# Kernel tuning notes

Hardware: AMD Instinct MI355X
Metric: run time of the kernel (lower is better)

Reference implementation:

```python
import jax, jax.numpy as jnp
from jax import lax
import numpy as np

# Model hyperparameters (match init_kwargs)
NUM_STEPS = 6
N_ETYPES = 8
D_IN = 128
D_OUT = 128
B, N, E = 32, 1024, 262144  # graphs, nodes per graph, total edges


def setup_inputs() -> dict:
    key = jax.random.key(0)
    ks = jax.random.split(key, 24)
    s = 0.05  # param scale for numeric stability over 6 GRU steps
    inp = {
        "h": jax.random.normal(ks[0], (B, N, D_IN), jnp.float32),
        "src": jax.random.randint(ks[1], (E,), 0, B * N, jnp.int32),
        "dst": jax.random.randint(ks[2], (E,), 0, B * N, jnp.int32),
        "etype": jax.random.randint(ks[3], (E,), 0, N_ETYPES, jnp.int32),
        "W_msg": jax.random.normal(ks[4], (N_ETYPES, D_OUT, D_OUT), jnp.float32) * s,
        "b_msg": jax.random.normal(ks[5], (N_ETYPES, D_OUT), jnp.float32) * s,
        "w_ih": jax.random.normal(ks[6], (3 * D_OUT, D_OUT), jnp.float32) * s,
        "w_hh": jax.random.normal(ks[7], (3 * D_OUT, D_OUT), jnp.float32) * s,
        "b_ih": jax.random.normal(ks[8], (3 * D_OUT,), jnp.float32) * s,
        "b_hh": jax.random.normal(ks[9], (3 * D_OUT,), jnp.float32) * s,
        "conv1_w": jax.random.normal(ks[10], (D_OUT, D_OUT, 3), jnp.float32) * s,
        "conv1_b": jax.random.normal(ks[11], (D_OUT,), jnp.float32) * s,
        "conv2_w": jax.random.normal(ks[12], (D_OUT, D_OUT, 1), jnp.float32) * s,
        "conv2_b": jax.random.normal(ks[13], (D_OUT,), jnp.float32) * s,
        "cc1_w": jax.random.normal(ks[14], (D_IN + D_OUT, D_IN + D_OUT, 3), jnp.float32) * s,
        "cc1_b": jax.random.normal(ks[15], (D_IN + D_OUT,), jnp.float32) * s,
        "cc2_w": jax.random.normal(ks[16], (D_IN + D_OUT, D_IN + D_OUT, 1), jnp.float32) * s,
        "cc2_b": jax.random.normal(ks[17], (D_IN + D_OUT,), jnp.float32) * s,
        "mlp_y_w": jax.random.normal(ks[18], (1, D_OUT), jnp.float32) * s,
        "mlp_y_b": jax.random.normal(ks[19], (1,), jnp.float32) * s,
        "mlp_z_w": jax.random.normal(ks[20], (1, D_IN + D_OUT), jnp.float32) * s,
        "mlp_z_b": jax.random.normal(ks[21], (1,), jnp.float32) * s,
    }
    return inp


def _conv1d(x, w, b):
    # x: [B, C_in, L], w: [C_out, C_in, K]
    y = lax.conv_general_dilated(x, w, (1,), "VALID",
                                 dimension_numbers=("NCW", "OIW", "NCW"))
    return y + b[None, :, None]


def _maxpool1d(x, k, stride):
    return lax.reduce_window(x, -jnp.inf, lax.max,
                             (1, 1, k), (1, 1, stride), "VALID")


def _ggnn(h0, src, dst, etype, W_msg, b_msg, w_ih, w_hh, b_ih, b_hh):
    # h0: [BN, D_OUT] (in_feats == out_feats so no zero-padding needed)
    n_nodes = h0.shape[0]

    def step(h, _):
        # transform each node by every etype weight: [BN, T, O]
        t = jnp.einsum("nd,tod->nto", h, W_msg) + b_msg
        m = t[src, etype]                                   # [E, O] gather
        a = jax.ops.segment_sum(m, dst, num_segments=n_nodes)  # scatter-add
        # torch.nn.GRUCell(a, h)
        gi = a @ w_ih.T + b_ih
        gh = h @ w_hh.T + b_hh
        i_r, i_z, i_n = jnp.split(gi, 3, axis=-1)
        h_r, h_z, h_n = jnp.split(gh, 3, axis=-1)
        r = jax.nn.sigmoid(i_r + h_r)
        z = jax.nn.sigmoid(i_z + h_z)
        n = jnp.tanh(i_n + r * h_n)
        return (1.0 - z) * n + z * h, None

    h_final, _ = lax.scan(step, h0, None, length=NUM_STEPS)
    return h_final


def reference(h, src, dst, etype, W_msg, b_msg, w_ih, w_hh, b_ih, b_hh,
              conv1_w, conv1_b, conv2_w, conv2_b, cc1_w, cc1_b, cc2_w, cc2_b,
              mlp_y_w, mlp_y_b, mlp_z_w, mlp_z_b):
    b, n, d = h.shape
    x = h.reshape(b * n, d)
    h_next = _ggnn(x, src, dst, etype, W_msg, b_msg, w_ih, w_hh, b_ih, b_hh)
    h_i = h_next.reshape(b, n, -1)                   # [B, N, O]
    c_i = jnp.concatenate([h_i, h], axis=-1)          # [B, N, O+D]

    Y_1 = _maxpool1d(jax.nn.relu(_conv1d(h_i.transpose(0, 2, 1), conv1_w, conv1_b)), 3, 2)
    Y_2 = _maxpool1d(jax.nn.relu(_conv1d(Y_1, conv2_w, conv2_b)), 2, 2).transpose(0, 2, 1)
    Z_1 = _maxpool1d(jax.nn.relu(_conv1d(c_i.transpose(0, 2, 1), cc1_w, cc1_b)), 3, 2)
    Z_2 = _maxpool1d(jax.nn.relu(_conv1d(Z_1, cc2_w, cc2_b)), 2, 2).transpose(0, 2, 1)

    before_avg = (Y_2 @ mlp_y_w.T + mlp_y_b) * (Z_2 @ mlp_z_w.T + mlp_z_b)  # [B, L, 1]
    avg = before_avg.mean(axis=1)                     # [B, 1]
    return jax.nn.sigmoid(avg).squeeze(-1)            # [B]
```

## Files before the change

kernel.cpp:

```cpp
#include <hip/hip_runtime.h>
#include <math.h>

#define BB 32
#define NNODE 1024
#define BN 32768
#define NE 262144
#define DD 128
#define NT 8
#define NSTEPS 6

typedef __attribute__((ext_vector_type(8))) short bf16x8;
typedef __attribute__((ext_vector_type(4))) float f32x4;

static __device__ __forceinline__ float4 ld4(const float* p) { return *(const float4*)p; }
static __device__ __forceinline__ float sigmoidf_(float x) { return 1.f / (1.f + expf(-x)); }
static __device__ __forceinline__ unsigned f2b(float f) {
    unsigned u = __float_as_uint(f);
    return (u + 0x7FFFu + ((u >> 16) & 1u)) >> 16;
}
static __device__ __forceinline__ float b2f(unsigned short b) {
    return __uint_as_float(((unsigned)b) << 16);
}
static __device__ __forceinline__ unsigned pk(float a, float b) {
    return f2b(a) | (f2b(b) << 16);
}
static __device__ __forceinline__ unsigned bmax2(unsigned a, unsigned b) {
    unsigned ah = a & 0xFFFF0000u, bh = b & 0xFFFF0000u;
    unsigned al = a & 0x0000FFFFu, bl = b & 0x0000FFFFu;
    return (ah > bh ? ah : bh) | (al > bl ? al : bl);
}
static __device__ __forceinline__ uint4 bmax4(uint4 a, uint4 b) {
    return make_uint4(bmax2(a.x, b.x), bmax2(a.y, b.y), bmax2(a.z, b.z), bmax2(a.w, b.w));
}

static constexpr size_t OFF_HCUR = 0;
static constexpr size_t OFF_HBF  = OFF_HCUR + (size_t)BN * DD * 4;
static constexpr size_t OFF_CNT  = OFF_HBF  + (size_t)BN * DD * 2;
static constexpr size_t OFF_DOFF = OFF_CNT  + (size_t)BN * NT * 4;
static constexpr size_t OFF_DBLK = OFF_DOFF + (size_t)BN * 4;
static constexpr size_t OFF_VTOF = OFF_DBLK + 512;
static constexpr size_t OFF_VTCU = OFF_VTOF + (size_t)BN * NT * 4;
static constexpr size_t OFF_SRC2 = OFF_VTCU + (size_t)BN * NT * 4;
static constexpr size_t OFF_WMB  = OFF_SRC2 + (size_t)NE * 4;
static constexpr size_t OFF_WIHB = OFF_WMB  + (size_t)NT * DD * DD * 2;
static constexpr size_t OFF_WHHB = OFF_WIHB + (size_t)3 * DD * DD * 2;
static constexpr size_t OFF_W1PY = OFF_WHHB + (size_t)3 * DD * DD * 2;
static constexpr size_t OFF_W1PZ = OFF_W1PY + (size_t)3 * 128 * 128 * 2;
static constexpr size_t OFF_W2YB = OFF_W1PZ + (size_t)3 * 256 * 256 * 2;
static constexpr size_t OFF_W2ZB = OFF_W2YB + (size_t)128 * 128 * 2;
static constexpr size_t OFF_ABF  = OFF_W2ZB + (size_t)256 * 256 * 2;
static constexpr size_t OFF_UN   = OFF_ABF  + (size_t)BN * DD * 2;
static constexpr size_t OFF_U1Y  = OFF_UN;
static constexpr size_t OFF_U1Z  = OFF_U1Y + (size_t)32 * 1024 * 128 * 2;
static constexpr size_t OFF_QY   = OFF_U1Z + (size_t)32 * 1024 * 256 * 2;
static constexpr size_t OFF_QZ   = OFF_QY  + (size_t)32 * 255 * 128 * 4;
static constexpr size_t WS_NEED  = OFF_QZ  + (size_t)32 * 255 * 256 * 4;

#define PREP_BLOCKS 5616
__global__ void k_prep(const float* __restrict__ h_in, float* __restrict__ hcur,
                       unsigned short* __restrict__ hbf,
                       const float* __restrict__ Wmsg, unsigned short* __restrict__ wmb,
                       const float* __restrict__ wih, unsigned short* __restrict__ wihb,
                       const float* __restrict__ whh, unsigned short* __restrict__ whhb,
                       const float* __restrict__ c2w, unsigned short* __restrict__ w2yb,
                       const float* __restrict__ z2w, unsigned short* __restrict__ w2zb,
                       const float* __restrict__ c1w, unsigned short* __restrict__ w1py,
                       const float* __restrict__ z1w, unsigned short* __restrict__ w1pz,
                       int* __restrict__ cnt)
{
    int blk = blockIdx.x, tid = threadIdx.x;
    if (blk < 4096) {
        int i = blk * 256 + tid;
        float4 v = ((const float4*)h_in)[i];
        ((float4*)hcur)[i] = v;
        ((uint2*)hbf)[i] = make_uint2(pk(v.x, v.y), pk(v.z, v.w));
    } else if (blk < 4224) {
        int i = (blk - 4096) * 256 + tid;
        float4 v = ((const float4*)Wmsg)[i];
        ((uint2*)wmb)[i] = make_uint2(pk(v.x, v.y), pk(v.z, v.w));
    } else if (blk < 4272) {
        int i = (blk - 4224) * 256 + tid;
        float4 v = ((const float4*)wih)[i];
        ((uint2*)wihb)[i] = make_uint2(pk(v.x, v.y), pk(v.z, v.w));
    } else if (blk < 4320) {
        int i = (blk - 4272) * 256 + tid;
        float4 v = ((const float4*)whh)[i];
        ((uint2*)whhb)[i] = make_uint2(pk(v.x, v.y), pk(v.z, v.w));
    } else if (blk < 4336) {
        int i = (blk - 4320) * 256 + tid;
        float4 v = ((const float4*)c2w)[i];
        ((uint2*)w2yb)[i] = make_uint2(pk(v.x, v.y), pk(v.z, v.w));
    } else if (blk < 4400) {
        int i = (blk - 4336) * 256 + tid;
        float4 v = ((const float4*)z2w)[i];
        ((uint2*)w2zb)[i] = make_uint2(pk(v.x, v.y), pk(v.z, v.w));
    } else if (blk < 4592) {
        int g = (blk - 4400) * 256 + tid;
        int k = g >> 14, rem = g & 16383;
        w1py[g] = (unsigned short)f2b(c1w[(size_t)rem * 3 + k]);
    } else if (blk < 5360) {
        int g = (blk - 4592) * 256 + tid;
        int k = g >> 16, rem = g & 65535;
        w1pz[g] = (unsigned short)f2b(z1w[(size_t)rem * 3 + k]);
    } else {
        ((uint4*)cnt)[(blk - 5360) * 256 + tid] = make_uint4(0, 0, 0, 0);
    }
}


__global__ void k_hist(const int* __restrict__ et, const int* __restrict__ dst,
                       int* __restrict__ cnt)
{
    int base = blockIdx.x * 1024, tid = threadIdx.x;
    for (int k = 0; k < 4; ++k) {
        int e = base + tid + k * 256;
        atomicAdd(&cnt[(size_t)dst[e] * NT + et[e]], 1);
    }
}

__global__ void k_degA(const int* __restrict__ cnt, int* __restrict__ doff,
                       int* __restrict__ dblk)
{
    __shared__ int ps[256];
    int tid = threadIdx.x;
    int v = blockIdx.x * 256 + tid;
    const int* cv = cnt + (size_t)v * NT;
    int d = 0;
#pragma unroll
    for (int t = 0; t < NT; ++t) d += cv[t];
    ps[tid] = d;
    __syncthreads();
    for (int off = 1; off < 256; off <<= 1) {
        int x = 0;
        if (tid >= off) x = ps[tid - off];
        __syncthreads();
        ps[tid] += x;
        __syncthreads();
    }
    doff[v] = ps[tid] - d;
    if (tid == 255) dblk[blockIdx.x] = ps[255];
}

__global__ void k_scan2(int* __restrict__ dblk)
{
    __shared__ int s[128];
    int tid = threadIdx.x;
    s[tid] = dblk[tid];
    __syncthreads();
    if (tid == 0) {
        int run = 0;
        for (int i = 0; i < 128; ++i) { int x = s[i]; s[i] = run; run += x; }
    }
    __syncthreads();
    dblk[tid] = s[tid];
}

__global__ void k_degB(const int* __restrict__ cnt, const int* __restrict__ doff,
                       const int* __restrict__ dblk,
                       int* __restrict__ vtoff, int* __restrict__ vtcur)
{
    int v = blockIdx.x * 256 + threadIdx.x;
    int run = doff[v] + dblk[blockIdx.x];
    const int* cv = cnt + (size_t)v * NT;
    int* vo = vtoff + (size_t)v * NT;
    int* vc = vtcur + (size_t)v * NT;
#pragma unroll
    for (int t = 0; t < NT; ++t) { vo[t] = run; vc[t] = run; run += cv[t]; }
}

__global__ void k_scatter(const int* __restrict__ src, const int* __restrict__ dst,
                          const int* __restrict__ et,
                          int* __restrict__ vtcur, int* __restrict__ ssrc2)
{
    int e = blockIdx.x * 256 + threadIdx.x;
    int slot = atomicAdd(&vtcur[(size_t)dst[e] * NT + et[e]], 1);
    ssrc2[slot] = src[e];
}


__launch_bounds__(256, 3)
__global__ void k_msgagg(const int* __restrict__ ssrc2, const int* __restrict__ vtoff,
                         const int* __restrict__ cnt,
                         const unsigned short* __restrict__ hbf,
                         const unsigned short* __restrict__ wmb,
                         const float* __restrict__ bmsg,
                         unsigned short* __restrict__ abf)
{
    __shared__ __align__(16) unsigned short As[64 * 128];
    __shared__ __align__(16) unsigned short Ws[128 * 128];
    __shared__ float bm[NT * DD];
    int m0 = blockIdx.x * 64;
    int tid = threadIdx.x;
    *(float4*)&bm[tid * 4] = ld4(bmsg + tid * 4);
    int lane = tid & 63, wv = tid >> 6;
    int wm = (wv >> 1) * 32, wn = (wv & 1) * 64;
    int lr = lane & 15, lk = lane >> 4;
    f32x4 acc[2][4];
#pragma unroll
    for (int i = 0; i < 2; ++i)
#pragma unroll
        for (int j = 0; j < 4; ++j) acc[i][j] = (f32x4){0.f, 0.f, 0.f, 0.f};

    int rA = tid >> 2, qA = tid & 3;
    unsigned bA = rA * 256 + qA * 64, swA = (rA & 7) << 4;
    int rW = tid >> 1, hW = tid & 1;
    unsigned bW = rW * 256 + hW * 128, swW = (rW & 7) << 4;
    int node = m0 + rA;

#pragma unroll
    for (int t = 0; t < NT; ++t) {
        __syncthreads();
        {
            int start = vtoff[(size_t)node * NT + t];
            int cv    = cnt[(size_t)node * NT + t];
            if (cv == 1) {
                const uint4* sp = (const uint4*)(hbf + (size_t)ssrc2[start] * DD + qA * 32);
#pragma unroll
                for (int c = 0; c < 4; ++c)
                    *(uint4*)((char*)As + ((bA + c * 16) ^ swA)) = sp[c];
            } else if (cv == 0) {
                uint4 z = make_uint4(0, 0, 0, 0);
#pragma unroll
                for (int c = 0; c < 4; ++c)
                    *(uint4*)((char*)As + ((bA + c * 16) ^ swA)) = z;
            } else {
                float ac[32];
#pragma unroll
                for (int j = 0; j < 32; ++j) ac[j] = 0.f;
                for (int i = 0; i < cv; ++i) {
                    const uint4* sp = (const uint4*)(hbf + (size_t)ssrc2[start + i] * DD + qA * 32);
#pragma unroll
                    for (int c = 0; c < 4; ++c) {
                        uint4 w = sp[c];
                        ac[c * 8 + 0] += b2f((unsigned short)(w.x & 0xFFFF));
                        ac[c * 8 + 1] += b2f((unsigned short)(w.x >> 16));
                        ac[c * 8 + 2] += b2f((unsigned short)(w.y & 0xFFFF));
                        ac[c * 8 + 3] += b2f((unsigned short)(w.y >> 16));
                        ac[c * 8 + 4] += b2f((unsigned short)(w.z & 0xFFFF));
                        ac[c * 8 + 5] += b2f((unsigned short)(w.z >> 16));
                        ac[c * 8 + 6] += b2f((unsigned short)(w.w & 0xFFFF));
                        ac[c * 8 + 7] += b2f((unsigned short)(w.w >> 16));
                    }
                }
#pragma unroll
                for (int c = 0; c < 4; ++c) {
                    uint4 o = make_uint4(pk(ac[c * 8 + 0], ac[c * 8 + 1]), pk(ac[c * 8 + 2], ac[c * 8 + 3]),
                                         pk(ac[c * 8 + 4], ac[c * 8 + 5]), pk(ac[c * 8 + 6], ac[c * 8 + 7]));
                    *(uint4*)((char*)As + ((bA + c * 16) ^ swA)) = o;
                }
            }
        }
        {
            const uint4* wp = (const uint4*)(wmb + ((size_t)t * DD + rW) * DD + hW * 64);
#pragma unroll
            for (int c = 0; c < 8; ++c)
                *(uint4*)((char*)Ws + ((bW + c * 16) ^ swW)) = wp[c];
        }
        __syncthreads();
#pragma unroll
        for (int kc = 0; kc < 4; ++kc) {
            int cb = kc * 64 + lk * 16;
            bf16x8 af[2], bfv[4];
#pragma unroll
            for (int mi = 0; mi < 2; ++mi) {
                int row = wm + mi * 16 + lr;
                af[mi] = *(const bf16x8*)((const char*)As + ((row * 256 + cb) ^ ((row & 7) << 4)));
            }
#pragma unroll
            for (int ni = 0; ni < 4; ++ni) {
                int row = wn + ni * 16 + lr;
                bfv[ni] = *(const bf16x8*)((const char*)Ws + ((row * 256 + cb) ^ ((row & 7) << 4)));
            }
#pragma unroll
            for (int mi = 0; mi < 2; ++mi)
#pragma unroll
                for (int ni = 0; ni < 4; ++ni)
                    acc[mi][ni] = __builtin_amdgcn_mfma_f32_16x16x32_bf16(af[mi], bfv[ni], acc[mi][ni], 0, 0, 0);
        }
    }
#pragma unroll
    for (int mi = 0; mi < 2; ++mi)
#pragma unroll
        for (int rg = 0; rg < 4; ++rg) {
            int v = m0 + wm + mi * 16 + lk * 4 + rg;
            const int* cvp = cnt + (size_t)v * NT;
            float c0 = (float)cvp[0], c1 = (float)cvp[1], c2 = (float)cvp[2], c3 = (float)cvp[3];
            float c4 = (float)cvp[4], c5 = (float)cvp[5], c6 = (float)cvp[6], c7 = (float)cvp[7];
#pragma unroll
            for (int ni = 0; ni < 4; ++ni) {
                int col = wn + ni * 16 + lr;
                float bias = c0 * bm[col] + c1 * bm[DD + col] + c2 * bm[2 * DD + col] + c3 * bm[3 * DD + col]
                           + c4 * bm[4 * DD + col] + c5 * bm[5 * DD + col] + c6 * bm[6 * DD + col] + c7 * bm[7 * DD + col];
                abf[(size_t)v * DD + col] = (unsigned short)f2b(acc[mi][ni][rg] + bias);
            }
        }
}


__launch_bounds__(512, 2)
__global__ void k_gru(const unsigned short* __restrict__ abf, float* __restrict__ h,
                      unsigned short* __restrict__ hbf,
                      const unsigned short* __restrict__ wihb, const unsigned short* __restrict__ whhb,
                      const float* __restrict__ bih, const float* __restrict__ bhh)
{
    __shared__ __align__(16) unsigned short Xs[128 * 128];
    __shared__ __align__(16) unsigned short Ws2[128 * 128];
    int m0 = blockIdx.x * 128;
    int tid = threadIdx.x;
    int lane = tid & 63, wv = tid >> 6;
    int wm = (wv >> 1) * 32, wn = (wv & 1) * 64;
    int lr = lane & 15, lk = lane >> 4;
    f32x4 aR[2][4], aZ[2][4], aI[2][4], aH[2][4];
#pragma unroll
    for (int i = 0; i < 2; ++i)
#pragma unroll
        for (int j = 0; j < 4; ++j) {
            aR[i][j] = (f32x4){0.f, 0.f, 0.f, 0.f};
            aZ[i][j] = (f32x4){0.f, 0.f, 0.f, 0.f};
            aI[i][j] = (f32x4){0.f, 0.f, 0.f, 0.f};
            aH[i][j] = (f32x4){0.f, 0.f, 0.f, 0.f};
        }
    int rx = tid >> 2, qx = tid & 3;
    unsigned bx = rx * 256 + qx * 64, swx = (rx & 7) << 4;
#pragma unroll
    for (int pass = 0; pass < 2; ++pass) {
        const unsigned short* X = pass ? hbf : abf;
        const unsigned short* W = pass ? whhb : wihb;
#pragma unroll
        for (int g = 0; g < 3; ++g) {
            __syncthreads();
            if (g == 0) {
                const uint4* sp = (const uint4*)(X + (size_t)(m0 + rx) * DD + qx * 32);
#pragma unroll
                for (int c = 0; c < 4; ++c)
                    *(uint4*)((char*)Xs + ((bx + c * 16) ^ swx)) = sp[c];
            }
            {
                const uint4* wp = (const uint4*)(W + (size_t)(g * DD + rx) * DD + qx * 32);
#pragma unroll
                for (int c = 0; c < 4; ++c)
                    *(uint4*)((char*)Ws2 + ((bx + c * 16) ^ swx)) = wp[c];
            }
            __syncthreads();
#pragma unroll
            for (int kc = 0; kc < 4; ++kc) {
                int cb = kc * 64 + lk * 16;
                bf16x8 af[2], bfv[4];
#pragma unroll
                for (int mi = 0; mi < 2; ++mi) {
                    int row = wm + mi * 16 + lr;
                    af[mi] = *(const bf16x8*)((const char*)Xs + ((row * 256 + cb) ^ ((row & 7) << 4)));
                }
#pragma unroll
                for (int ni = 0; ni < 4; ++ni) {
                    int row = wn + ni * 16 + lr;
                    bfv[ni] = *(const bf16x8*)((const char*)Ws2 + ((row * 256 + cb) ^ ((row & 7) << 4)));
                }
#pragma unroll
                for (int mi = 0; mi < 2; ++mi)
#pragma unroll
                    for (int ni = 0; ni < 4; ++ni) {
                        if (g == 0)
                            aR[mi][ni] = __builtin_amdgcn_mfma_f32_16x16x32_bf16(af[mi], bfv[ni], aR[mi][ni], 0, 0, 0);
                        else if (g == 1)
                            aZ[mi][ni] = __builtin_amdgcn_mfma_f32_16x16x32_bf16(af[mi], bfv[ni], aZ[mi][ni], 0, 0, 0);
                        else if (pass == 0)
                            aI[mi][ni] = __builtin_amdgcn_mfma_f32_16x16x32_bf16(af[mi], bfv[ni], aI[mi][ni], 0, 0, 0);
                        else
                            aH[mi][ni] = __builtin_amdgcn_mfma_f32_16x16x32_bf16(af[mi], bfv[ni], aH[mi][ni], 0, 0, 0);
                    }
            }
        }
    }
#pragma unroll
    for (int ni = 0; ni < 4; ++ni) {
        int col = wn + ni * 16 + lr;
        float br_ = bih[col] + bhh[col];
        float bz_ = bih[DD + col] + bhh[DD + col];
        float bin_ = bih[2 * DD + col], bhn_ = bhh[2 * DD + col];
#pragma unroll
        for (int mi = 0; mi < 2; ++mi)
#pragma unroll
            for (int rg = 0; rg < 4; ++rg) {
                int v = m0 + wm + mi * 16 + lk * 4 + rg;
                float rr = sigmoidf_(aR[mi][ni][rg] + br_);
                float zz = sigmoidf_(aZ[mi][ni][rg] + bz_);
                float nn = tanhf(aI[mi][ni][rg] + bin_ + rr * (aH[mi][ni][rg] + bhn_));
                float hold = h[(size_t)v * DD + col];
                float hnew = (1.f - zz) * nn + zz * hold;
                h[(size_t)v * DD + col] = hnew;
                hbf[(size_t)v * DD + col] = (unsigned short)f2b(hnew);
            }
    }
}


template <int CIN>
__launch_bounds__(256, 2)
__global__ void k_conv1m(const unsigned short* __restrict__ hbf, const float* __restrict__ h0,
                         const unsigned short* __restrict__ w1p, const float* __restrict__ bias,
                         unsigned short* __restrict__ U1)
{
    __shared__ __align__(16) unsigned short As[128 * 64];
    __shared__ __align__(16) unsigned short Ws[128 * 64];
    int p0 = blockIdx.x * 128, b = blockIdx.y, n0 = blockIdx.z * 128;
    int tid = threadIdx.x;
    int lane = tid & 63, wv = tid >> 6;
    int wm = (wv >> 1) * 64, wn = (wv & 1) * 64;
    int lr = lane & 15, lk = lane >> 4;
    f32x4 acc[4][4];
#pragma unroll
    for (int i = 0; i < 4; ++i)
#pragma unroll
        for (int j = 0; j < 4; ++j) acc[i][j] = (f32x4){0.f, 0.f, 0.f, 0.f};

    int r = tid >> 1, halfc = tid & 1;
    unsigned boff = r * 128 + halfc * 64;
    unsigned sw = (r & 7) << 4;
#pragma unroll
    for (int k = 0; k < 3; ++k) {
        for (int c0 = 0; c0 < CIN; c0 += 64) {
            __syncthreads();
            {
                int row = p0 + k + r; if (row > NNODE - 1) row = NNODE - 1;
                int ci = c0 + halfc * 32;
                if (CIN == 128 || ci < 128) {
                    const uint4* sp = (const uint4*)(hbf + ((size_t)(b * NNODE + row)) * DD + ci);
#pragma unroll
                    for (int c = 0; c < 4; ++c)
                        *(uint4*)((char*)As + ((boff + c * 16) ^ sw)) = sp[c];
                } else {
                    const float4* sp = (const float4*)(h0 + ((size_t)(b * NNODE + row)) * DD + (ci - 128));
#pragma unroll
                    for (int c = 0; c < 4; ++c) {
                        float4 v0 = sp[2 * c], v1 = sp[2 * c + 1];
                        *(uint4*)((char*)As + ((boff + c * 16) ^ sw)) =
                            make_uint4(pk(v0.x, v0.y), pk(v0.z, v0.w), pk(v1.x, v1.y), pk(v1.z, v1.w));
                    }
                }
            }
            {
                const uint4* wp = (const uint4*)(w1p + ((size_t)k * CIN + n0 + r) * CIN + c0 + halfc * 32);
#pragma unroll
                for (int c = 0; c < 4; ++c)
                    *(uint4*)((char*)Ws + ((boff + c * 16) ^ sw)) = wp[c];
            }
            __syncthreads();
#pragma unroll
            for (int kc = 0; kc < 2; ++kc) {
                int cb = kc * 64 + lk * 16;
                bf16x8 af[4], bfv[4];
#pragma unroll
                for (int mi = 0; mi < 4; ++mi) {
                    int row = wm + mi * 16 + lr;
                    af[mi] = *(const bf16x8*)((const char*)As + ((row * 128 + cb) ^ ((row & 7) << 4)));
                }
#pragma unroll
                for (int ni = 0; ni < 4; ++ni) {
                    int row = wn + ni * 16 + lr;
                    bfv[ni] = *(const bf16x8*)((const char*)Ws + ((row * 128 + cb) ^ ((row & 7) << 4)));
                }
#pragma unroll
                for (int mi = 0; mi < 4; ++mi)
#pragma unroll
                    for (int ni = 0; ni < 4; ++ni)
                        acc[mi][ni] = __builtin_amdgcn_mfma_f32_16x16x32_bf16(af[mi], bfv[ni], acc[mi][ni], 0, 0, 0);
            }
        }
    }
#pragma unroll
    for (int ni = 0; ni < 4; ++ni) {
        int co = n0 + wn + ni * 16 + lr;
        float bs = bias[co];
#pragma unroll
        for (int mi = 0; mi < 4; ++mi)
#pragma unroll
            for (int rg = 0; rg < 4; ++rg) {
                int pos = p0 + wm + mi * 16 + lk * 4 + rg;
                if (pos < NNODE - 2) {
                    float v = fmaxf(0.f, acc[mi][ni][rg] + bs);
                    U1[((size_t)b * NNODE + pos) * CIN + co] = (unsigned short)f2b(v);
                }
            }
    }
}


template <int CIN>
__launch_bounds__(256, 2)
__global__ void k_conv2m(const unsigned short* __restrict__ U1, const unsigned short* __restrict__ w2b,
                         const float* __restrict__ bias, float* __restrict__ Q)
{
    __shared__ __align__(16) unsigned short As[128 * 64];
    __shared__ __align__(16) unsigned short Ws[128 * 64];
    int m0 = blockIdx.x * 128, b = blockIdx.y, n0 = blockIdx.z * 128;
    int tid = threadIdx.x;
    int lane = tid & 63, wv = tid >> 6;
    int wm = (wv >> 1) * 64, wn = (wv & 1) * 64;
    int lr = lane & 15, lk = lane >> 4;
    f32x4 acc[4][4];
#pragma unroll
    for (int i = 0; i < 4; ++i)
#pragma unroll
        for (int j = 0; j < 4; ++j) acc[i][j] = (f32x4){0.f, 0.f, 0.f, 0.f};

    int r = tid >> 1, halfc = tid & 1;
    unsigned boff = r * 128 + halfc * 64;
    unsigned sw = (r & 7) << 4;
    for (int c0 = 0; c0 < CIN; c0 += 64) {
        __syncthreads();
        {
            int pr = 2 * (m0 + r);
            int r0 = pr, r1 = pr + 1, r2v = pr + 2;
            if (r2v > NNODE - 1) r2v = NNODE - 1;
            if (r1 > NNODE - 1) r1 = NNODE - 1;
            int ci = c0 + halfc * 32;
            const unsigned short* bp = U1 + (size_t)b * NNODE * CIN + ci;
            const uint4* p0q = (const uint4*)(bp + (size_t)r0 * CIN);
            const uint4* p1q = (const uint4*)(bp + (size_t)r1 * CIN);
            const uint4* p2q = (const uint4*)(bp + (size_t)r2v * CIN);
#pragma unroll
            for (int c = 0; c < 4; ++c) {
                uint4 mm = bmax4(bmax4(p0q[c], p1q[c]), p2q[c]);
                *(uint4*)((char*)As + ((boff + c * 16) ^ sw)) = mm;
            }
        }
        {
            const uint4* wp = (const uint4*)(w2b + (size_t)(n0 + r) * CIN + c0 + halfc * 32);
#pragma unroll
            for (int c = 0; c < 4; ++c)
                *(uint4*)((char*)Ws + ((boff + c * 16) ^ sw)) = wp[c];
        }
        __syncthreads();
#pragma unroll
        for (int kc = 0; kc < 2; ++kc) {
            int cb = kc * 64 + lk * 16;
            bf16x8 af[4], bfv[4];
#pragma unroll
            for (int mi = 0; mi < 4; ++mi) {
                int row = wm + mi * 16 + lr;
                af[mi] = *(const bf16x8*)((const char*)As + ((row * 128 + cb) ^ ((row & 7) << 4)));
            }
#pragma unroll
            for (int ni = 0; ni < 4; ++ni) {
                int row = wn + ni * 16 + lr;
                bfv[ni] = *(const bf16x8*)((const char*)Ws + ((row * 128 + cb) ^ ((row & 7) << 4)));
            }
#pragma unroll
            for (int mi = 0; mi < 4; ++mi)
#pragma unroll
                for (int ni = 0; ni < 4; ++ni)
                    acc[mi][ni] = __builtin_amdgcn_mfma_f32_16x16x32_bf16(af[mi], bfv[ni], acc[mi][ni], 0, 0, 0);
        }
    }
#pragma unroll
    for (int ni = 0; ni < 4; ++ni) {
        int co = n0 + wn + ni * 16 + lr;
        float bs = bias[co];
#pragma unroll
        for (int mi = 0; mi < 4; ++mi) {
            int l0 = m0 + wm + mi * 16 + lk * 4;
            float v0 = fmaxf(0.f, acc[mi][ni][0] + bs);
            float v1 = fmaxf(0.f, acc[mi][ni][1] + bs);
            float v2 = fmaxf(0.f, acc[mi][ni][2] + bs);
            float v3 = fmaxf(0.f, acc[mi][ni][3] + bs);
            int jq = l0 >> 1;
            if (jq < 255)     Q[((size_t)b * 255 + jq) * CIN + co]     = fmaxf(v0, v1);
            if (jq + 1 < 255) Q[((size_t)b * 255 + jq + 1) * CIN + co] = fmaxf(v2, v3);
        }
    }
}


__launch_bounds__(256)
__global__ void k_final(const float* __restrict__ QY, const float* __restrict__ QZ,
                        const float* __restrict__ wy, const float* __restrict__ by,
                        const float* __restrict__ wz, const float* __restrict__ bz,
                        float* __restrict__ out)
{
    int b = blockIdx.x, tid = threadIdx.x;
    float p = 0.f;
    if (tid < 255) {
        const float* qy = QY + ((size_t)(b * 255 + tid)) * 128;
        const float* qz = QZ + ((size_t)(b * 255 + tid)) * 256;
        float dy = 0.f, dz = 0.f;
        for (int c = 0; c < 128; c += 4) {
            float4 q = ld4(qy + c), wv = ld4(wy + c);
            dy += q.x * wv.x + q.y * wv.y + q.z * wv.z + q.w * wv.w;
        }
        for (int c = 0; c < 256; c += 4) {
            float4 q = ld4(qz + c), wv = ld4(wz + c);
            dz += q.x * wv.x + q.y * wv.y + q.z * wv.z + q.w * wv.w;
        }
        p = (dy + by[0]) * (dz + bz[0]);
    }
    __shared__ float red[4];
    for (int off = 32; off > 0; off >>= 1) p += __shfl_down(p, off);
    if ((tid & 63) == 0) red[tid >> 6] = p;
    __syncthreads();
    if (tid == 0) {
        float s = red[0] + red[1] + red[2] + red[3];
        out[b] = 1.f / (1.f + expf(-s / 255.f));
    }
}


extern "C" void kernel_launch(void* const* d_in, const int* in_sizes, int n_in,
                              void* d_out, int out_size, void* d_ws, size_t ws_size,
                              hipStream_t stream)
{
    const float* h_in = (const float*)d_in[0];
    const int* src = (const int*)d_in[1];
    const int* dst = (const int*)d_in[2];
    const int* et  = (const int*)d_in[3];
    const float* Wmsg = (const float*)d_in[4];
    const float* bmsg = (const float*)d_in[5];
    const float* wih = (const float*)d_in[6];
    const float* whh = (const float*)d_in[7];
    const float* bih = (const float*)d_in[8];
    const float* bhh = (const float*)d_in[9];
    const float* c1w = (const float*)d_in[10];
    const float* c1b = (const float*)d_in[11];
    const float* c2w = (const float*)d_in[12];
    const float* c2b = (const float*)d_in[13];
    const float* z1w = (const float*)d_in[14];
    const float* z1b = (const float*)d_in[15];
    const float* z2w = (const float*)d_in[16];
    const float* z2b = (const float*)d_in[17];
    const float* wy  = (const float*)d_in[18];
    const float* by  = (const float*)d_in[19];
    const float* wz  = (const float*)d_in[20];
    const float* bz  = (const float*)d_in[21];
    float* out = (float*)d_out;

    if (ws_size < WS_NEED) return;

    char* ws = (char*)d_ws;
    float* hcur = (float*)(ws + OFF_HCUR);
    unsigned short* hbf  = (unsigned short*)(ws + OFF_HBF);
    int*   cnt   = (int*)(ws + OFF_CNT);
    int*   doff  = (int*)(ws + OFF_DOFF);
    int*   dblk  = (int*)(ws + OFF_DBLK);
    int*   vtoff = (int*)(ws + OFF_VTOF);
    int*   vtcur = (int*)(ws + OFF_VTCU);
    int*   ssrc2 = (int*)(ws + OFF_SRC2);
    unsigned short* wmb  = (unsigned short*)(ws + OFF_WMB);
    unsigned short* wihb = (unsigned short*)(ws + OFF_WIHB);
    unsigned short* whhb = (unsigned short*)(ws + OFF_WHHB);
    unsigned short* w1py = (unsigned short*)(ws + OFF_W1PY);
    unsigned short* w1pz = (unsigned short*)(ws + OFF_W1PZ);
    unsigned short* w2yb = (unsigned short*)(ws + OFF_W2YB);
    unsigned short* w2zb = (unsigned short*)(ws + OFF_W2ZB);
    unsigned short* abf  = (unsigned short*)(ws + OFF_ABF);
    unsigned short* U1Y  = (unsigned short*)(ws + OFF_U1Y);
    unsigned short* U1Z  = (unsigned short*)(ws + OFF_U1Z);
    float* QY   = (float*)(ws + OFF_QY);
    float* QZ   = (float*)(ws + OFF_QZ);

    k_prep<<<PREP_BLOCKS, 256, 0, stream>>>(h_in, hcur, hbf, Wmsg, wmb, wih, wihb, whh, whhb,
                                            c2w, w2yb, z2w, w2zb, c1w, w1py, z1w, w1pz, cnt);

    k_hist<<<256, 256, 0, stream>>>(et, dst, cnt);
    k_degA<<<128, 256, 0, stream>>>(cnt, doff, dblk);
    k_scan2<<<1, 128, 0, stream>>>(dblk);
    k_degB<<<128, 256, 0, stream>>>(cnt, doff, dblk, vtoff, vtcur);
    k_scatter<<<1024, 256, 0, stream>>>(src, dst, et, vtcur, ssrc2);

    for (int s = 0; s < NSTEPS; ++s) {
        k_msgagg<<<BN / 64, 256, 0, stream>>>(ssrc2, vtoff, cnt, hbf, wmb, bmsg, abf);
        k_gru<<<BN / 128, 512, 0, stream>>>(abf, hcur, hbf, wihb, whhb, bih, bhh);
    }

    k_conv1m<128><<<dim3(8, 32, 1), 256, 0, stream>>>(hbf, h_in, w1py, c1b, U1Y);
    k_conv2m<128><<<dim3(4, 32, 1), 256, 0, stream>>>(U1Y, w2yb, c2b, QY);
    k_conv1m<256><<<dim3(8, 32, 2), 256, 0, stream>>>(hbf, h_in, w1pz, z1b, U1Z);
    k_conv2m<256><<<dim3(4, 32, 2), 256, 0, stream>>>(U1Z, w2zb, z2b, QZ);
    k_final<<<32, 256, 0, stream>>>(QY, QZ, wy, by, wz, bz, out);
}
```

Baseline: 611.7 us.

## Halve msgagg node tile and prefetch per-type edge sources up front

The message-aggregation kernel now handles 32 nodes per block instead of 64, with 8 threads per node row, and launches twice as many blocks. Before the type loop it loads all per-type offsets and counts as vector loads, then prefetches the first two source indices per type. This is meant to raise parallelism and hide the latency of the dependent gather loads. The cost is that each block reloads the full per-type weight matrices for half as many rows, which doubles weight traffic per node, and register pressure goes up.

```diff
diff --git a/kernel.cpp b/kernel.cpp
--- a/kernel.cpp
+++ b/kernel.cpp
@@ -31,6 +31,16 @@
 }
 static __device__ __forceinline__ uint4 bmax4(uint4 a, uint4 b) {
     return make_uint4(bmax2(a.x, b.x), bmax2(a.y, b.y), bmax2(a.z, b.z), bmax2(a.w, b.w));
+}
+static __device__ __forceinline__ void upacc(float* ac, uint4 w0, uint4 w1) {
+    ac[0] += b2f((unsigned short)(w0.x & 0xFFFF)); ac[1] += b2f((unsigned short)(w0.x >> 16));
+    ac[2] += b2f((unsigned short)(w0.y & 0xFFFF)); ac[3] += b2f((unsigned short)(w0.y >> 16));
+    ac[4] += b2f((unsigned short)(w0.z & 0xFFFF)); ac[5] += b2f((unsigned short)(w0.z >> 16));
+    ac[6] += b2f((unsigned short)(w0.w & 0xFFFF)); ac[7] += b2f((unsigned short)(w0.w >> 16));
+    ac[8] += b2f((unsigned short)(w1.x & 0xFFFF)); ac[9] += b2f((unsigned short)(w1.x >> 16));
+    ac[10] += b2f((unsigned short)(w1.y & 0xFFFF)); ac[11] += b2f((unsigned short)(w1.y >> 16));
+    ac[12] += b2f((unsigned short)(w1.z & 0xFFFF)); ac[13] += b2f((unsigned short)(w1.z >> 16));
+    ac[14] += b2f((unsigned short)(w1.w & 0xFFFF)); ac[15] += b2f((unsigned short)(w1.w >> 16));
 }
 
 static constexpr size_t OFF_HCUR = 0;
@@ -186,68 +196,74 @@
                          const float* __restrict__ bmsg,
                          unsigned short* __restrict__ abf)
 {
-    __shared__ __align__(16) unsigned short As[64 * 128];
+    __shared__ __align__(16) unsigned short As[32 * 128];
     __shared__ __align__(16) unsigned short Ws[128 * 128];
     __shared__ float bm[NT * DD];
-    int m0 = blockIdx.x * 64;
+    int m0 = blockIdx.x * 32;
     int tid = threadIdx.x;
     *(float4*)&bm[tid * 4] = ld4(bmsg + tid * 4);
     int lane = tid & 63, wv = tid >> 6;
-    int wm = (wv >> 1) * 32, wn = (wv & 1) * 64;
+    int wm = (wv >> 1) * 16, wn = (wv & 1) * 64;
     int lr = lane & 15, lk = lane >> 4;
-    f32x4 acc[2][4];
-#pragma unroll
-    for (int i = 0; i < 2; ++i)
-#pragma unroll
-        for (int j = 0; j < 4; ++j) acc[i][j] = (f32x4){0.f, 0.f, 0.f, 0.f};
-
-    int rA = tid >> 2, qA = tid & 3;
-    unsigned bA = rA * 256 + qA * 64, swA = (rA & 7) << 4;
+    f32x4 acc[4];
+#pragma unroll
+    for (int j = 0; j < 4; ++j) acc[j] = (f32x4){0.f, 0.f, 0.f, 0.f};
+
+    int rA = tid >> 3, qA = tid & 7;
+    unsigned bA = rA * 256 + qA * 32, swA = (rA & 7) << 4;
     int rW = tid >> 1, hW = tid & 1;
     unsigned bW = rW * 256 + hW * 128, swW = (rW & 7) << 4;
     int node = m0 + rA;
 
+    int vt[NT], cn[NT];
+    {
+        uint4 a0 = *(const uint4*)(vtoff + (size_t)node * NT);
+        uint4 a1 = *(const uint4*)(vtoff + (size_t)node * NT + 4);
+        vt[0] = a0.x; vt[1] = a0.y; vt[2] = a0.z; vt[3] = a0.w;
+        vt[4] = a1.x; vt[5] = a1.y; vt[6] = a1.z; vt[7] = a1.w;
+        uint4 c0 = *(const uint4*)(cnt + (size_t)node * NT);
+        uint4 c1 = *(const uint4*)(cnt + (size_t)node * NT + 4);
+        cn[0] = c0.x; cn[1] = c0.y; cn[2] = c0.z; cn[3] = c0.w;
+        cn[4] = c1.x; cn[5] = c1.y; cn[6] = c1.z; cn[7] = c1.w;
+    }
+    int s0[NT], s1[NT];
+#pragma unroll
+    for (int t = 0; t < NT; ++t) {
+        s0[t] = (cn[t] > 0) ? ssrc2[vt[t]] : 0;
+        s1[t] = (cn[t] > 1) ? ssrc2[vt[t] + 1] : 0;
+    }
+
 #pragma unroll
     for (int t = 0; t < NT; ++t) {
         __syncthreads();
         {
-            int start = vtoff[(size_t)node * NT + t];
-            int cv    = cnt[(size_t)node * NT + t];
+            int cv = cn[t];
             if (cv == 1) {
-                const uint4* sp = (const uint4*)(hbf + (size_t)ssrc2[start] * DD + qA * 32);
-#pragma unroll
-                for (int c = 0; c < 4; ++c)
-                    *(uint4*)((char*)As + ((bA + c * 16) ^ swA)) = sp[c];
+                const uint4* sp = (const uint4*)(hbf + (size_t)s0[t] * DD + qA * 16);
+                uint4 w0 = sp[0], w1 = sp[1];
+                *(uint4*)((char*)As + (bA ^ swA)) = w0;
+                *(uint4*)((char*)As + ((bA + 16) ^ swA)) = w1;
             } else if (cv == 0) {
                 uint4 z = make_uint4(0, 0, 0, 0);
-#pragma unroll
-                for (int c = 0; c < 4; ++c)
-                    *(uint4*)((char*)As + ((bA + c * 16) ^ swA)) = z;
+                *(uint4*)((char*)As + (bA ^ swA)) = z;
+                *(uint4*)((char*)As + ((bA + 16) ^ swA)) = z;
             } else {
-                float ac[32];
-#pragma unroll
-                for (int j = 0; j < 32; ++j) ac[j] = 0.f;
-                for (int i = 0; i < cv; ++i) {
-                    const uint4* sp = (const uint4*)(hbf + (size_t)ssrc2[start + i] * DD + qA * 32);
-#pragma unroll
-                    for (int c = 0; c < 4; ++c) {
-                        uint4 w = sp[c];
-                        ac[c * 8 + 0] += b2f((unsigned short)(w.x & 0xFFFF));
-                        ac[c * 8 + 1] += b2f((unsigned short)(w.x >> 16));
-                        ac[c * 8 + 2] += b2f((unsigned short)(w.y & 0xFFFF));
-                        ac[c * 8 + 3] += b2f((unsigned short)(w.y >> 16));
-                        ac[c * 8 + 4] += b2f((unsigned short)(w.z & 0xFFFF));
-                        ac[c * 8 + 5] += b2f((unsigned short)(w.z >> 16));
-                        ac[c * 8 + 6] += b2f((unsigned short)(w.w & 0xFFFF));
-                        ac[c * 8 + 7] += b2f((unsigned short)(w.w >> 16));
-                    }
+                const uint4* p0 = (const uint4*)(hbf + (size_t)s0[t] * DD + qA * 16);
+                const uint4* p1 = (const uint4*)(hbf + (size_t)s1[t] * DD + qA * 16);
+                float ac[16];
+#pragma unroll
+                for (int j = 0; j < 16; ++j) ac[j] = 0.f;
+                upacc(ac, p0[0], p0[1]);
+                upacc(ac, p1[0], p1[1]);
+                for (int i = 2; i < cv; ++i) {
+                    int s = ssrc2[vt[t] + i];
+                    const uint4* pp = (const uint4*)(hbf + (size_t)s * DD + qA * 16);
+                    upacc(ac, pp[0], pp[1]);
                 }
-#pragma unroll
-                for (int c = 0; c < 4; ++c) {
-                    uint4 o = make_uint4(pk(ac[c * 8 + 0], ac[c * 8 + 1]), pk(ac[c * 8 + 2], ac[c * 8 + 3]),
-                                         pk(ac[c * 8 + 4], ac[c * 8 + 5]), pk(ac[c * 8 + 6], ac[c * 8 + 7]));
-                    *(uint4*)((char*)As + ((bA + c * 16) ^ swA)) = o;
-                }
+                uint4 o0 = make_uint4(pk(ac[0], ac[1]), pk(ac[2], ac[3]), pk(ac[4], ac[5]), pk(ac[6], ac[7]));
+                uint4 o1 = make_uint4(pk(ac[8], ac[9]), pk(ac[10], ac[11]), pk(ac[12], ac[13]), pk(ac[14], ac[15]));
+                *(uint4*)((char*)As + (bA ^ swA)) = o0;
+                *(uint4*)((char*)As + ((bA + 16) ^ swA)) = o1;
             }
         }
         {
@@ -260,40 +276,33 @@
 #pragma unroll
         for (int kc = 0; kc < 4; ++kc) {
             int cb = kc * 64 + lk * 16;
-            bf16x8 af[2], bfv[4];
-#pragma unroll
-            for (int mi = 0; mi < 2; ++mi) {
-                int row = wm + mi * 16 + lr;
-                af[mi] = *(const bf16x8*)((const char*)As + ((row * 256 + cb) ^ ((row & 7) << 4)));
-            }
+            int rowA = wm + lr;
+            bf16x8 af = *(const bf16x8*)((const char*)As + ((rowA * 256 + cb) ^ ((rowA & 7) << 4)));
+            bf16x8 bfv[4];
 #pragma unroll
             for (int ni = 0; ni < 4; ++ni) {
                 int row = wn + ni * 16 + lr;
                 bfv[ni] = *(const bf16x8*)((const char*)Ws + ((row * 256 + cb) ^ ((row & 7) << 4)));
             }
 #pragma unroll
-            for (int mi = 0; mi < 2; ++mi)
-#pragma unroll
-                for (int ni = 0; ni < 4; ++ni)
-                    acc[mi][ni] = __builtin_amdgcn_mfma_f32_16x16x32_bf16(af[mi], bfv[ni], acc[mi][ni], 0, 0, 0);
-        }
-    }
-#pragma unroll
-    for (int mi = 0; mi < 2; ++mi)
-#pragma unroll
-        for (int rg = 0; rg < 4; ++rg) {
-            int v = m0 + wm + mi * 16 + lk * 4 + rg;
-            const int* cvp = cnt + (size_t)v * NT;
-            float c0 = (float)cvp[0], c1 = (float)cvp[1], c2 = (float)cvp[2], c3 = (float)cvp[3];
-            float c4 = (float)cvp[4], c5 = (float)cvp[5], c6 = (float)cvp[6], c7 = (float)cvp[7];
-#pragma unroll
-            for (int ni = 0; ni < 4; ++ni) {
-                int col = wn + ni * 16 + lr;
-                float bias = c0 * bm[col] + c1 * bm[DD + col] + c2 * bm[2 * DD + col] + c3 * bm[3 * DD + col]
-                           + c4 * bm[4 * DD + col] + c5 * bm[5 * DD + col] + c6 * bm[6 * DD + col] + c7 * bm[7 * DD + col];
-                abf[(size_t)v * DD + col] = (unsigned short)f2b(acc[mi][ni][rg] + bias);
-            }
-        }
+            for (int ni = 0; ni < 4; ++ni)
+                acc[ni] = __builtin_amdgcn_mfma_f32_16x16x32_bf16(af, bfv[ni], acc[ni], 0, 0, 0);
+        }
+    }
+#pragma unroll
+    for (int rg = 0; rg < 4; ++rg) {
+        int v = m0 + wm + lk * 4 + rg;
+        const int* cvp = cnt + (size_t)v * NT;
+        float c0 = (float)cvp[0], c1 = (float)cvp[1], c2 = (float)cvp[2], c3 = (float)cvp[3];
+        float c4 = (float)cvp[4], c5 = (float)cvp[5], c6 = (float)cvp[6], c7 = (float)cvp[7];
+#pragma unroll
+        for (int ni = 0; ni < 4; ++ni) {
+            int col = wn + ni * 16 + lr;
+            float bias = c0 * bm[col] + c1 * bm[DD + col] + c2 * bm[2 * DD + col] + c3 * bm[3 * DD + col]
+                       + c4 * bm[4 * DD + col] + c5 * bm[5 * DD + col] + c6 * bm[6 * DD + col] + c7 * bm[7 * DD + col];
+            abf[(size_t)v * DD + col] = (unsigned short)f2b(acc[ni][rg] + bias);
+        }
+    }
 }
 
 
@@ -667,7 +676,7 @@
     k_scatter<<<1024, 256, 0, stream>>>(src, dst, et, vtcur, ssrc2);
 
     for (int s = 0; s < NSTEPS; ++s) {
-        k_msgagg<<<BN / 64, 256, 0, stream>>>(ssrc2, vtoff, cnt, hbf, wmb, bmsg, abf);
+        k_msgagg<<<BN / 32, 256, 0, stream>>>(ssrc2, vtoff, cnt, hbf, wmb, bmsg, abf);
         k_gru<<<BN / 128, 512, 0, stream>>>(abf, hcur, hbf, wihb, whhb, bih, bhh);
     }
 
```

After: 721.8 us. 1.18x slower.
